# Performance work log

Measured on AMD Instinct MI355X. Metric: run time of the kernel, lower is better.

The kernel has to match this reference:

```python
import math
import jax, jax.numpy as jnp
import numpy as np

B, S, HID, NH = 1, 2048, 4096, 32
HD = HID // NH  # 128
INV_NORM = 1.0 / math.sqrt(HD)


def _build_alibi(n_heads, seq_len, batch):
    # Standard Bloom ALiBi slopes.
    cp2 = 2 ** math.floor(math.log2(n_heads))
    base = 2.0 ** (-(2.0 ** -(math.log2(cp2) - 3)))
    slopes = base ** np.arange(1, cp2 + 1)
    if cp2 != n_heads:
        extra_base = 2.0 ** (-(2.0 ** -(math.log2(2 * cp2) - 3)))
        n_rem = min(cp2, n_heads - cp2)
        slopes = np.concatenate([slopes, extra_base ** np.arange(1, 2 * n_rem + 1, 2)])
    arange = np.arange(seq_len, dtype=np.float32)[None, None, :]
    alibi = slopes[:, None, None].astype(np.float32) * arange  # [NH,1,S]
    alibi = np.broadcast_to(alibi[None], (batch, n_heads, 1, seq_len)).reshape(batch * n_heads, 1, seq_len)
    return jnp.asarray(alibi, jnp.float32)


def setup_inputs() -> dict:
    key = jax.random.key(0)
    ks = jax.random.split(key, 5)
    return {
        "hidden_states": jax.random.normal(ks[0], (B, S, HID), jnp.float32),
        "alibi": _build_alibi(NH, S, B),  # [B*NH, 1, S]
        "w_qkv": jax.random.normal(ks[1], (3 * HID, HID), jnp.float32) * 0.02,
        "b_qkv": jax.random.normal(ks[2], (3 * HID,), jnp.float32) * 0.02,
        "w_dense": jax.random.normal(ks[3], (HID, HID), jnp.float32) * 0.02,
        "b_dense": jax.random.normal(ks[4], (HID,), jnp.float32) * 0.02,
    }


def reference(hidden_states, alibi, w_qkv, b_qkv, w_dense, b_dense):
    b, s, _ = hidden_states.shape
    # Fused QKV projection, per-head interleaved layout [B,S,NH,3,HD]
    fused = hidden_states @ w_qkv.T + b_qkv
    fused = fused.reshape(b, s, NH, 3, HD)
    q = fused[..., 0, :].transpose(0, 2, 1, 3).reshape(b * NH, s, HD)
    k = fused[..., 1, :].transpose(0, 2, 1, 3).reshape(b * NH, s, HD)
    v = fused[..., 2, :].transpose(0, 2, 1, 3).reshape(b * NH, s, HD)
    # baddbmm(alibi, q, k^T, beta=1.0, alpha=inv_norm_factor)
    scores = alibi + INV_NORM * jnp.einsum("bqd,bkd->bqk", q, k)  # [B*NH,S,S]
    causal = jnp.tril(jnp.ones((s, s), dtype=bool))
    scores = jnp.where(causal[None], scores, jnp.finfo(scores.dtype).min)
    probs = jax.nn.softmax(scores.astype(jnp.float32), axis=-1).astype(hidden_states.dtype)
    ctx = jnp.einsum("bqk,bkd->bqd", probs, v)  # [B*NH,S,HD]
    ctx = ctx.reshape(b, NH, s, HD).transpose(0, 2, 1, 3).reshape(b, s, HID)
    return ctx @ w_dense.T + b_dense
```

## Files before the change

### kernel.cpp

```cpp
#include <hip/hip_runtime.h>
#include <math.h>


typedef __attribute__((ext_vector_type(8))) short short8;
typedef __attribute__((ext_vector_type(4))) float floatx4;
typedef __attribute__((ext_vector_type(4))) unsigned short ushort4v;

#define S_LEN 2048
#define HID_DIM 4096
#define NHEADS 32
#define HDIM 128
#define QKV_N 12288
#define QK_STRIDE 8192
#define INV_NORM 0.08838834764831845f

__device__ __forceinline__ unsigned short f2bf(float f) {
    union { float f; unsigned int i; } v; v.f = f;
    unsigned int u = v.i;
    return (unsigned short)((u + 0x7fffu + ((u >> 16) & 1u)) >> 16);
}

typedef __attribute__((address_space(1))) unsigned int guint;
typedef __attribute__((address_space(3))) unsigned int luint;
__device__ __forceinline__ void gl_lds16(const unsigned short* g, unsigned short* l) {
    __builtin_amdgcn_global_load_lds((guint*)g, (luint*)l, 16, 0, 0);
}

__global__ __launch_bounds__(256) void cvt_bf16(
    const float* __restrict__ src, unsigned short* __restrict__ dst)
{
    size_t i = ((size_t)blockIdx.x * 256 + threadIdx.x) * 8;
    float4 x = *(const float4*)(src + i);
    float4 y = *(const float4*)(src + i + 4);
    union { unsigned u[4]; short8 s; } r;
    r.u[0] = (unsigned)f2bf(x.x) | ((unsigned)f2bf(x.y) << 16);
    r.u[1] = (unsigned)f2bf(x.z) | ((unsigned)f2bf(x.w) << 16);
    r.u[2] = (unsigned)f2bf(y.x) | ((unsigned)f2bf(y.y) << 16);
    r.u[3] = (unsigned)f2bf(y.z) | ((unsigned)f2bf(y.w) << 16);
    *(short8*)(dst + i) = r.s;
}

template <int MODE>
__global__ __launch_bounds__(256) void gemm_bt(
    const unsigned short* __restrict__ A,
    const unsigned short* __restrict__ B,
    const float* __restrict__ bias,
    unsigned short* __restrict__ Cq,
    float* __restrict__ Cf,
    unsigned short* __restrict__ vt,
    int M, int N, int K)
{
    __shared__ unsigned short a_lds[128 * 64];
    __shared__ unsigned short b_lds[128 * 64];
    int t = threadIdx.x;
    int w = t >> 6, lane = t & 63, quad = lane >> 4, l15 = lane & 15;
    int mb = blockIdx.y * 128, nb = blockIdx.x * 128;
    int wm = (w >> 1) * 64, wn = (w & 1) * 64;

    int lr = lane >> 3;
    int lcol = ((lane & 7) ^ lr) * 8;
    const unsigned short* pa = A + (size_t)(mb + w * 32 + lr) * K + lcol;
    const unsigned short* pb = B + (size_t)(nb + w * 32 + lr) * K + lcol;
    unsigned short* la = &a_lds[(w * 32) * 64];
    unsigned short* lb = &b_lds[(w * 32) * 64];

    floatx4 acc[4][4];
    for (int i = 0; i < 4; i++)
        for (int j = 0; j < 4; j++) acc[i][j] = (floatx4)0.0f;

    for (int k0 = 0; k0 < K; k0 += 64) {
        for (int it = 0; it < 4; it++) {
            gl_lds16(pa + k0 + (size_t)it * 8 * K, la + it * 8 * 64);
            gl_lds16(pb + k0 + (size_t)it * 8 * K, lb + it * 8 * 64);
        }
        __syncthreads();
        for (int ks = 0; ks < 2; ks++) {
            short8 af[4], bfr[4];
            for (int i = 0; i < 4; i++) {
                int r = wm + i * 16 + l15;
                af[i] = *(const short8*)&a_lds[r * 64 + (((ks * 4 + quad) ^ (l15 & 7)) * 8)];
            }
            for (int j = 0; j < 4; j++) {
                int r = wn + j * 16 + l15;
                bfr[j] = *(const short8*)&b_lds[r * 64 + (((ks * 4 + quad) ^ (l15 & 7)) * 8)];
            }
            for (int i = 0; i < 4; i++)
                for (int j = 0; j < 4; j++)
                    acc[i][j] = __builtin_amdgcn_mfma_f32_16x16x32_bf16(af[i], bfr[j], acc[i][j], 0, 0, 0);
        }
        __syncthreads();
    }

    if (MODE == 1) {
        int type = blockIdx.x % 3;
        int h = blockIdx.x / 3;
        if (type == 2) {
            for (int j = 0; j < 4; j++) {
                int local = wn + j * 16 + l15;
                float bv = bias[nb + local];
                unsigned short* vp = vt + ((size_t)h * HDIM + local) * S_LEN;
                for (int i = 0; i < 4; i++) {
                    int rowbase = mb + wm + i * 16 + quad * 4;
                    ushort4v pk;
                    for (int r = 0; r < 4; r++) pk[r] = f2bf(acc[i][j][r] + bv);
                    *(ushort4v*)&vp[rowbase] = pk;
                }
            }
        } else {
            size_t colbase = (size_t)h * 256 + type * 128;
            for (int j = 0; j < 4; j++) {
                int local = wn + j * 16 + l15;
                float bv = bias[nb + local];
                for (int i = 0; i < 4; i++) {
                    int rowbase = mb + wm + i * 16 + quad * 4;
                    for (int r = 0; r < 4; r++)
                        Cq[(size_t)(rowbase + r) * QK_STRIDE + colbase + local] =
                            f2bf(acc[i][j][r] + bv);
                }
            }
        }
    } else {
        for (int j = 0; j < 4; j++) {
            int col = nb + wn + j * 16 + l15;
            float bv = bias[col];
            for (int i = 0; i < 4; i++) {
                int rowbase = mb + wm + i * 16 + quad * 4;
                for (int r = 0; r < 4; r++)
                    Cf[(size_t)(rowbase + r) * N + col] = acc[i][j][r] + bv;
            }
        }
    }
}

__global__ __launch_bounds__(256) void attn_flash(
    const unsigned short* __restrict__ qk,
    const unsigned short* __restrict__ vt,
    const float* __restrict__ alibi,
    unsigned short* __restrict__ ctx)
{
    __shared__ unsigned short k_lds[64 * 136];
    __shared__ unsigned short vt_lds[128 * 72];
    __shared__ unsigned short p_lds[4 * 16 * 72];

    int h = blockIdx.x;
    int qb = blockIdx.y * 64;
    int t = threadIdx.x;
    int w = t >> 6, lane = t & 63, quad = lane >> 4, l15 = lane & 15;
    int qoff = h * 256;

    short8 qf[4];
    {
        int qrow = qb + w * 16 + l15;
        const unsigned short* qp = qk + (size_t)qrow * QK_STRIDE + qoff;
        for (int ks = 0; ks < 4; ks++)
            qf[ks] = *(const short8*)&qp[ks * 32 + quad * 8];
    }

    floatx4 o[8];
    for (int j = 0; j < 8; j++) o[j] = (floatx4)0.0f;
    float m_prev[4], l_prev[4];
    for (int r = 0; r < 4; r++) { m_prev[r] = -INFINITY; l_prev[r] = 0.0f; }

    int ntiles = qb / 64 + 1;
    for (int tile = 0; tile < ntiles; tile++) {
        int kb = tile * 64;
        for (int i = 0; i < 4; i++) {
            int idx = t + 256 * i;
            int krow = idx >> 4, kcol = (idx & 15) * 8;
            *(short8*)&k_lds[krow * 136 + kcol] =
                *(const short8*)(qk + (size_t)(kb + krow) * QK_STRIDE + qoff + 128 + kcol);
            int d = idx >> 3, ch = (idx & 7) * 8;
            *(short8*)&vt_lds[d * 72 + ch] =
                *(const short8*)(vt + ((size_t)h * HDIM + d) * S_LEN + kb + ch);
        }
        __syncthreads();

        floatx4 s[4];
        for (int j = 0; j < 4; j++) s[j] = (floatx4)0.0f;
        for (int ks = 0; ks < 4; ks++) {
            for (int j = 0; j < 4; j++) {
                short8 bfr = *(const short8*)&k_lds[(j * 16 + l15) * 136 + ks * 32 + quad * 8];
                s[j] = __builtin_amdgcn_mfma_f32_16x16x32_bf16(qf[ks], bfr, s[j], 0, 0, 0);
            }
        }

        float sv[4][4];
        for (int j = 0; j < 4; j++) {
            int kcol = kb + j * 16 + l15;
            float al = alibi[h * S_LEN + kcol];
            for (int r = 0; r < 4; r++) {
                int qrow = qb + w * 16 + quad * 4 + r;
                float x = s[j][r] * INV_NORM + al;
                sv[j][r] = (kcol <= qrow) ? x : -INFINITY;
            }
        }

        float p[4][4];
        for (int r = 0; r < 4; r++) {
            float mt = fmaxf(fmaxf(sv[0][r], sv[1][r]), fmaxf(sv[2][r], sv[3][r]));
            for (int off = 1; off < 16; off <<= 1)
                mt = fmaxf(mt, __shfl_xor(mt, off, 64));
            float m_new = fmaxf(m_prev[r], mt);
            float alpha = __expf(m_prev[r] - m_new);
            float rs = 0.0f;
            for (int j = 0; j < 4; j++) {
                float pv = __expf(sv[j][r] - m_new);
                p[j][r] = pv;
                rs += pv;
            }
            for (int off = 1; off < 16; off <<= 1)
                rs += __shfl_xor(rs, off, 64);
            l_prev[r] = l_prev[r] * alpha + rs;
            m_prev[r] = m_new;
            for (int j = 0; j < 8; j++) o[j][r] *= alpha;
        }

        {
            unsigned short* pb = &p_lds[w * 16 * 72];
            for (int j = 0; j < 4; j++)
                for (int r = 0; r < 4; r++)
                    pb[(quad * 4 + r) * 72 + j * 16 + l15] = f2bf(p[j][r]);
        }
        {
            const unsigned short* pb = &p_lds[w * 16 * 72];
            for (int ks = 0; ks < 2; ks++) {
                short8 ap = *(const short8*)&pb[l15 * 72 + ks * 32 + quad * 8];
                for (int j = 0; j < 8; j++) {
                    short8 bv = *(const short8*)&vt_lds[(j * 16 + l15) * 72 + ks * 32 + quad * 8];
                    o[j] = __builtin_amdgcn_mfma_f32_16x16x32_bf16(ap, bv, o[j], 0, 0, 0);
                }
            }
        }
        __syncthreads();
    }

    for (int r = 0; r < 4; r++) {
        float linv = 1.0f / l_prev[r];
        int qrow = qb + w * 16 + quad * 4 + r;
        unsigned short* op = ctx + (size_t)qrow * HID_DIM + h * HDIM;
        for (int j = 0; j < 8; j++)
            op[j * 16 + l15] = f2bf(o[j][r] * linv);
    }
}

extern "C" void kernel_launch(void* const* d_in, const int* in_sizes, int n_in,
                              void* d_out, int out_size, void* d_ws, size_t ws_size,
                              hipStream_t stream) {
    const float* hidden  = (const float*)d_in[0];
    const float* alibi   = (const float*)d_in[1];
    const float* w_qkv   = (const float*)d_in[2];
    const float* b_qkv   = (const float*)d_in[3];
    const float* w_dense = (const float*)d_in[4];
    const float* b_dense = (const float*)d_in[5];
    float* out = (float*)d_out;

    unsigned short* ws    = (unsigned short*)d_ws;
    unsigned short* wq_bf = ws;
    unsigned short* fused = ws + (size_t)50331648;
    unsigned short* vt    = fused + (size_t)S_LEN * QK_STRIDE;
    unsigned short* hbf   = vt + (size_t)NHEADS * HDIM * S_LEN;
    unsigned short* ctx   = hbf;
    unsigned short* wd_bf = wq_bf;

    dim3 blk(256);
    cvt_bf16<<<dim3(4096),  blk, 0, stream>>>(hidden,  hbf);
    cvt_bf16<<<dim3(24576), blk, 0, stream>>>(w_qkv,   wq_bf);
    gemm_bt<1><<<dim3(QKV_N / 128, S_LEN / 128), blk, 0, stream>>>(
        hbf, wq_bf, b_qkv, fused, nullptr, vt, S_LEN, QKV_N, HID_DIM);
    attn_flash<<<dim3(NHEADS, S_LEN / 64), blk, 0, stream>>>(fused, vt, alibi, ctx);
    cvt_bf16<<<dim3(8192), blk, 0, stream>>>(w_dense, wd_bf);
    gemm_bt<0><<<dim3(HID_DIM / 128, S_LEN / 128), blk, 0, stream>>>(
        ctx, wd_bf, b_dense, nullptr, out, nullptr, S_LEN, HID_DIM, HID_DIM);
}
```

Measured before the change: 851.5 us.

## Replace GEMM with 4-stage pipelined 512-thread kernel using larger tiles

```diff
diff --git a/kernel.cpp b/kernel.cpp
--- a/kernel.cpp
+++ b/kernel.cpp
@@ -24,6 +24,17 @@
 typedef __attribute__((address_space(3))) unsigned int luint;
 __device__ __forceinline__ void gl_lds16(const unsigned short* g, unsigned short* l) {
     __builtin_amdgcn_global_load_lds((guint*)g, (luint*)l, 16, 0, 0);
+}
+
+__device__ __forceinline__ void wvm8() { asm volatile("s_waitcnt vmcnt(8)" ::: "memory"); }
+__device__ __forceinline__ void wvm6() { asm volatile("s_waitcnt vmcnt(6)" ::: "memory"); }
+__device__ __forceinline__ void wvm4() { asm volatile("s_waitcnt vmcnt(4)" ::: "memory"); }
+__device__ __forceinline__ void wvm3() { asm volatile("s_waitcnt vmcnt(3)" ::: "memory"); }
+__device__ __forceinline__ void wvm0() { asm volatile("s_waitcnt vmcnt(0)" ::: "memory"); }
+
+__device__ __forceinline__ void phase_bar() {
+    __builtin_amdgcn_s_barrier();
+    __builtin_amdgcn_sched_barrier(0);
 }
 
 __global__ __launch_bounds__(256) void cvt_bf16(
@@ -40,8 +51,8 @@
     *(short8*)(dst + i) = r.s;
 }
 
-template <int MODE>
-__global__ __launch_bounds__(256) void gemm_bt(
+template <int MODE, int BM>
+__global__ __launch_bounds__(512, 2) void gemm_pipe(
     const unsigned short* __restrict__ A,
     const unsigned short* __restrict__ B,
     const float* __restrict__ bias,
@@ -50,83 +61,129 @@
     unsigned short* __restrict__ vt,
     int M, int N, int K)
 {
-    __shared__ unsigned short a_lds[128 * 64];
-    __shared__ unsigned short b_lds[128 * 64];
-    int t = threadIdx.x;
-    int w = t >> 6, lane = t & 63, quad = lane >> 4, l15 = lane & 15;
-    int mb = blockIdx.y * 128, nb = blockIdx.x * 128;
-    int wm = (w >> 1) * 64, wn = (w & 1) * 64;
-
-    int lr = lane >> 3;
-    int lcol = ((lane & 7) ^ lr) * 8;
-    const unsigned short* pa = A + (size_t)(mb + w * 32 + lr) * K + lcol;
-    const unsigned short* pb = B + (size_t)(nb + w * 32 + lr) * K + lcol;
-    unsigned short* la = &a_lds[(w * 32) * 64];
-    unsigned short* lb = &b_lds[(w * 32) * 64];
-
-    floatx4 acc[4][4];
-    for (int i = 0; i < 4; i++)
+    constexpr int BN = 256;
+    constexpr int BK = 32;
+    constexpr int MF = BM / 32;
+    constexpr int WR = BM / 2;
+    constexpr int BUFSH = (BM + BN) * BK;
+    constexpr int LA = (BM * BK * 2) / 8192;
+
+    __shared__ unsigned short lds[4 * BUFSH];
+
+    const int t = threadIdx.x;
+    const int w = t >> 6, lane = t & 63, quad = lane >> 4, l15 = lane & 15;
+    const int wr = w >> 2, wc = w & 3;
+
+    const int gx = gridDim.x;
+    const int nwg = gx * gridDim.y;
+    const int wg = blockIdx.y * gx + blockIdx.x;
+    const int swz = (wg & 7) * (nwg >> 3) + (wg >> 3);
+    const int bx = swz % gx, by = swz / gx;
+    const int mb = by * BM, nb = bx * BN;
+
+    const int srow = w * 16 + (lane >> 2);
+    const int schunk = (((lane & 3) ^ ((lane >> 2) & 3)) << 3);
+    const unsigned short* pa = A + (size_t)(mb + srow) * K + schunk;
+    const unsigned short* pb = B + (size_t)(nb + srow) * K + schunk;
+    const int la_off = w * 512;
+    const int lb_off = BM * BK + w * 512;
+
+    const int fchunk = ((quad ^ (l15 & 3)) << 3);
+    const int aoff = (wr * WR + l15) * BK + fchunk;
+    const int boff = BM * BK + (wc * 64 + l15) * BK + fchunk;
+
+    floatx4 acc[MF][4];
+#pragma unroll
+    for (int i = 0; i < MF; i++)
+#pragma unroll
         for (int j = 0; j < 4; j++) acc[i][j] = (floatx4)0.0f;
 
-    for (int k0 = 0; k0 < K; k0 += 64) {
-        for (int it = 0; it < 4; it++) {
-            gl_lds16(pa + k0 + (size_t)it * 8 * K, la + it * 8 * 64);
-            gl_lds16(pb + k0 + (size_t)it * 8 * K, lb + it * 8 * 64);
-        }
-        __syncthreads();
-        for (int ks = 0; ks < 2; ks++) {
-            short8 af[4], bfr[4];
-            for (int i = 0; i < 4; i++) {
-                int r = wm + i * 16 + l15;
-                af[i] = *(const short8*)&a_lds[r * 64 + (((ks * 4 + quad) ^ (l15 & 7)) * 8)];
-            }
-            for (int j = 0; j < 4; j++) {
-                int r = wn + j * 16 + l15;
-                bfr[j] = *(const short8*)&b_lds[r * 64 + (((ks * 4 + quad) ^ (l15 & 7)) * 8)];
-            }
-            for (int i = 0; i < 4; i++)
-                for (int j = 0; j < 4; j++)
-                    acc[i][j] = __builtin_amdgcn_mfma_f32_16x16x32_bf16(af[i], bfr[j], acc[i][j], 0, 0, 0);
-        }
-        __syncthreads();
-    }
+    int kstage = 0;
+    auto stage = [&](int bufi) {
+        unsigned short* lb = &lds[bufi * BUFSH];
+#pragma unroll
+        for (int i = 0; i < LA; i++)
+            gl_lds16(pa + kstage + (size_t)i * 128 * K, lb + la_off + i * 4096);
+        gl_lds16(pb + kstage, lb + lb_off);
+        gl_lds16(pb + kstage + (size_t)128 * K, lb + lb_off + 4096);
+        kstage += BK;
+    };
+    auto compute = [&](int bufi) {
+        const unsigned short* lt = &lds[bufi * BUFSH];
+        short8 af[MF], bfr[4];
+#pragma unroll
+        for (int m = 0; m < MF; m++)
+            af[m] = *(const short8*)&lt[aoff + m * 16 * BK];
+#pragma unroll
+        for (int n = 0; n < 4; n++)
+            bfr[n] = *(const short8*)&lt[boff + n * 16 * BK];
+        __builtin_amdgcn_s_setprio(1);
+#pragma unroll
+        for (int m = 0; m < MF; m++)
+#pragma unroll
+            for (int n = 0; n < 4; n++)
+                acc[m][n] = __builtin_amdgcn_mfma_f32_16x16x32_bf16(af[m], bfr[n], acc[m][n], 0, 0, 0);
+        __builtin_amdgcn_s_setprio(0);
+    };
+
+    const int NT = K / BK;
+
+    stage(0); stage(1); stage(2);
+
+    for (int kt = 0; kt < NT - 2; kt++) {
+        if constexpr (BM == 256) wvm8(); else wvm6();
+        phase_bar();
+        if (kt < NT - 3) stage((kt + 3) & 3);
+        compute(kt & 3);
+    }
+    if constexpr (BM == 256) wvm4(); else wvm3();
+    phase_bar();
+    compute((NT - 2) & 3);
+    wvm0();
+    phase_bar();
+    compute((NT - 1) & 3);
 
     if (MODE == 1) {
-        int type = blockIdx.x % 3;
-        int h = blockIdx.x / 3;
-        if (type == 2) {
-            for (int j = 0; j < 4; j++) {
-                int local = wn + j * 16 + l15;
-                float bv = bias[nb + local];
-                unsigned short* vp = vt + ((size_t)h * HDIM + local) * S_LEN;
-                for (int i = 0; i < 4; i++) {
-                    int rowbase = mb + wm + i * 16 + quad * 4;
+#pragma unroll
+        for (int j = 0; j < 4; j++) {
+            int cb = nb + wc * 64 + j * 16;
+            int h = cb / 384;
+            int type = (cb >> 7) % 3;
+            int db = cb & 127;
+            float bv = bias[cb + l15];
+            if (type == 2) {
+                unsigned short* vp = vt + ((size_t)h * HDIM + db + l15) * S_LEN;
+#pragma unroll
+                for (int m = 0; m < MF; m++) {
+                    int rowbase = mb + wr * WR + m * 16 + quad * 4;
                     ushort4v pk;
-                    for (int r = 0; r < 4; r++) pk[r] = f2bf(acc[i][j][r] + bv);
+#pragma unroll
+                    for (int r = 0; r < 4; r++) pk[r] = f2bf(acc[m][j][r] + bv);
                     *(ushort4v*)&vp[rowbase] = pk;
                 }
-            }
-        } else {
-            size_t colbase = (size_t)h * 256 + type * 128;
-            for (int j = 0; j < 4; j++) {
-                int local = wn + j * 16 + l15;
-                float bv = bias[nb + local];
-                for (int i = 0; i < 4; i++) {
-                    int rowbase = mb + wm + i * 16 + quad * 4;
+            } else {
+                size_t colo = (size_t)h * 256 + type * 128 + db + l15;
+#pragma unroll
+                for (int m = 0; m < MF; m++) {
+                    int rowbase = mb + wr * WR + m * 16 + quad * 4;
+#pragma unroll
                     for (int r = 0; r < 4; r++)
-                        Cq[(size_t)(rowbase + r) * QK_STRIDE + colbase + local] =
-                            f2bf(acc[i][j][r] + bv);
+                        Cq[(size_t)(rowbase + r) * QK_STRIDE + colo] =
+                            f2bf(acc[m][j][r] + bv);
                 }
             }
         }
     } else {
+#pragma unroll
         for (int j = 0; j < 4; j++) {
-            int col = nb + wn + j * 16 + l15;
+            int col = nb + wc * 64 + j * 16 + l15;
             float bv = bias[col];
-            for (int i = 0; i < 4; i++) {
-                int rowbase = mb + wm + i * 16 + quad * 4;
+#pragma unroll
+            for (int m = 0; m < MF; m++) {
+                int rowbase = mb + wr * WR + m * 16 + quad * 4;
+#pragma unroll
                 for (int r = 0; r < 4; r++)
-                    Cf[(size_t)(rowbase + r) * N + col] = acc[i][j][r] + bv;
+                    Cf[(size_t)(rowbase + r) * N + col] = acc[m][j][r] + bv;
             }
         }
     }
@@ -262,13 +319,13 @@
     unsigned short* ctx   = hbf;
     unsigned short* wd_bf = wq_bf;
 
-    dim3 blk(256);
+    dim3 blk(256), blk512(512);
     cvt_bf16<<<dim3(4096),  blk, 0, stream>>>(hidden,  hbf);
     cvt_bf16<<<dim3(24576), blk, 0, stream>>>(w_qkv,   wq_bf);
-    gemm_bt<1><<<dim3(QKV_N / 128, S_LEN / 128), blk, 0, stream>>>(
+    gemm_pipe<1, 256><<<dim3(QKV_N / 256, S_LEN / 256), blk512, 0, stream>>>(
         hbf, wq_bf, b_qkv, fused, nullptr, vt, S_LEN, QKV_N, HID_DIM);
     attn_flash<<<dim3(NHEADS, S_LEN / 64), blk, 0, stream>>>(fused, vt, alibi, ctx);
     cvt_bf16<<<dim3(8192), blk, 0, stream>>>(w_dense, wd_bf);
-    gemm_bt<0><<<dim3(HID_DIM / 128, S_LEN / 128), blk, 0, stream>>>(
+    gemm_pipe<0, 128><<<dim3(HID_DIM / 256, S_LEN / 128), blk512, 0, stream>>>(
         ctx, wd_bf, b_dense, nullptr, out, nullptr, S_LEN, HID_DIM, HID_DIM);
 }
```

Result: faster. 795.0 us (-6.6%).
